# Optimization experiments

Hardware: AMD Instinct MI355X
Metric: run time of the kernel (lower is better)

The kernel has to match this reference:

```python
import jax, jax.numpy as jnp
import numpy as np

D_MODEL = 1024
HEADS = 16
D_K = D_MODEL // HEADS

def setup_inputs() -> dict:
    key = jax.random.key(0)
    ks = jax.random.split(key, 12)
    B, S = 4, 2048
    sc = 1.0 / np.sqrt(D_MODEL)
    inp = {
        'q': jax.random.normal(ks[0], (B, S, D_MODEL), jnp.float32),
        'k': jax.random.normal(ks[1], (B, S, D_MODEL), jnp.float32),
        'v': jax.random.normal(ks[2], (B, S, D_MODEL), jnp.float32),
        'mask': jnp.ones((B, S, S), jnp.int32),
        'Wq': jax.random.normal(ks[3], (D_MODEL, D_MODEL), jnp.float32) * sc,
        'bq': jnp.zeros((D_MODEL,), jnp.float32),
        'Wk': jax.random.normal(ks[4], (D_MODEL, D_MODEL), jnp.float32) * sc,
        'bk': jnp.zeros((D_MODEL,), jnp.float32),
        'Wv': jax.random.normal(ks[5], (D_MODEL, D_MODEL), jnp.float32) * sc,
        'bv': jnp.zeros((D_MODEL,), jnp.float32),
        'Wo': jax.random.normal(ks[6], (D_MODEL, D_MODEL), jnp.float32) * sc,
        'bo': jnp.zeros((D_MODEL,), jnp.float32),
    }
    return inp

def _proj_heads(x, W, b):
    # torch Linear: y = x @ W.T + b; then view(B,S,h,dk).transpose(1,2) -> [B,h,S,dk]
    B, S, _ = x.shape
    y = jnp.einsum('bsd,ed->bse', x, W) + b
    return y.reshape(B, S, HEADS, D_K).transpose(0, 2, 1, 3)

def reference(q, k, v, mask, Wq, bq, Wk, bk, Wv, bv, Wo, bo):
    B, S, _ = q.shape
    qh = _proj_heads(q, Wq, bq)  # [B,h,S,dk]
    kh = _proj_heads(k, Wk, bk)
    vh = _proj_heads(v, Wv, bv)
    scores = jnp.einsum('bhqd,bhkd->bhqk', qh, kh) / np.sqrt(D_K)
    scores = jnp.where(mask[:, None, :, :] == 0, jnp.float32(-1e9), scores)
    probs = jax.nn.softmax(scores, axis=-1)  # dropout = identity (eval mode)
    ctx = jnp.einsum('bhqk,bhkd->bhqd', probs, vh)
    concat = ctx.transpose(0, 2, 1, 3).reshape(B, S, D_MODEL)
    return jnp.einsum('bsd,ed->bse', concat, Wo) + bo
```

## Files before the change

kernel.cpp:

```cpp
#include <hip/hip_runtime.h>
#include <stdint.h>

#define DM 1024
#define SQL 2048
#define NB 4
#define NH 16
#define DK 64

typedef unsigned short u16;
typedef unsigned int u32;
typedef float f32x4 __attribute__((ext_vector_type(4)));
typedef short s16x8 __attribute__((ext_vector_type(8)));
typedef unsigned int u32x2 __attribute__((ext_vector_type(2)));

__device__ __forceinline__ u16 f2bf(float x) {
  union { float f; u32 u; } un; un.f = x;
  return (u16)((un.u + 0x8000u) >> 16);
}
__device__ __forceinline__ u32 pack_bf16(float a, float b) {
  union { float f; u32 u; } ua, ub; ua.f = a; ub.f = b;
  return ((ua.u + 0x8000u) >> 16) | ((ub.u + 0x8000u) & 0xFFFF0000u);
}

typedef __attribute__((address_space(3))) u32 lds_u32_t;
typedef __attribute__((address_space(1))) u32 g_u32_t;

__device__ __forceinline__ void async_cp16(void* lds, const void* g) {
  __builtin_amdgcn_global_load_lds((g_u32_t*)(unsigned long long)g,
                                   (lds_u32_t*)(unsigned long long)lds,
                                   16, 0, 0);
}

__device__ __forceinline__ void mfma16(f32x4& c, s16x8 a, s16x8 b) {
  c = __builtin_amdgcn_mfma_f32_16x16x32_bf16(a, b, c, 0, 0, 0);
}

__global__ void init_flag_k(int* flag) { if (threadIdx.x == 0) *flag = 1; }

__device__ __forceinline__ void store_bf4(u16* dst, float4 v) {
  u32 lo = pack_bf16(v.x, v.y);
  u32 hi = pack_bf16(v.z, v.w);
  ((u32*)dst)[0] = lo; ((u32*)dst)[1] = hi;
}

__global__ void __launch_bounds__(256) convert_scan_k(
    const float* __restrict__ q, const float* __restrict__ k, const float* __restrict__ v,
    const float* __restrict__ wq, const float* __restrict__ wk,
    const float* __restrict__ wv, const float* __restrict__ wo,
    const int* __restrict__ mask,
    u16* qb, u16* kb, u16* vb, u16* wqb, u16* wkb, u16* wvb, u16* wob, int* flag)
{
  const size_t i = (size_t)blockIdx.x * 256 + threadIdx.x;
  const size_t i4 = i * 4;
  store_bf4(qb + i4, *(const float4*)(q + i4));
  store_bf4(kb + i4, *(const float4*)(k + i4));
  store_bf4(vb + i4, *(const float4*)(v + i4));
  if (i4 < 1048576) {
    store_bf4(wqb + i4, *(const float4*)(wq + i4));
    store_bf4(wkb + i4, *(const float4*)(wk + i4));
    store_bf4(wvb + i4, *(const float4*)(wv + i4));
    store_bf4(wob + i4, *(const float4*)(wo + i4));
  }
  const size_t mi = i * 8;
  int4 m0 = *(const int4*)(mask + mi);
  int4 m1 = *(const int4*)(mask + mi + 4);
  bool z = (m0.x == 0) | (m0.y == 0) | (m0.z == 0) | (m0.w == 0) |
           (m1.x == 0) | (m1.y == 0) | (m1.z == 0) | (m1.w == 0);
  if (z) *flag = 0;
}

__device__ __forceinline__ void gemm_core(const u16* __restrict__ A, const u16* __restrict__ W,
                                          int m0, int n0, u16* sA, u16* sB, f32x4 (&acc)[4][4])
{
  const int tid = threadIdx.x;
  const int l = tid & 63, w = tid >> 6;
  const int g = l >> 4, ln = l & 15;
  const int wm = w & 1, wn = w >> 1;

  for (int kt = 0; kt < DM; kt += 64) {
#pragma unroll
    for (int i = 0; i < 4; ++i) {
      int s = w * 256 + i * 64 + l;
      int m = s >> 3;
      int kc = (s & 7) ^ (m & 7);
      async_cp16(sA + (size_t)(w * 256 + i * 64) * 8,
                 A + (size_t)(m0 + m) * DM + kt + kc * 8);
    }
#pragma unroll
    for (int i = 0; i < 4; ++i) {
      int s = w * 256 + i * 64 + l;
      int n = s >> 3;
      int kc = (s & 7) ^ (n & 7);
      async_cp16(sB + (size_t)(w * 256 + i * 64) * 8,
                 W + (size_t)(n0 + n) * DM + kt + kc * 8);
    }
    asm volatile("s_waitcnt vmcnt(0)" ::: "memory");
    __syncthreads();
#pragma unroll
    for (int ks = 0; ks < 2; ++ks) {
      s16x8 af[4], bfr[4];
#pragma unroll
      for (int mt = 0; mt < 4; ++mt) {
        int m = wm * 64 + mt * 16 + ln;
        int slot = m * 8 + ((ks * 4 + g) ^ (m & 7));
        af[mt] = *(const s16x8*)(sA + (size_t)slot * 8);
      }
#pragma unroll
      for (int nt = 0; nt < 4; ++nt) {
        int n = wn * 64 + nt * 16 + ln;
        int slot = n * 8 + ((ks * 4 + g) ^ (n & 7));
        bfr[nt] = *(const s16x8*)(sB + (size_t)slot * 8);
      }
#pragma unroll
      for (int mt = 0; mt < 4; ++mt)
#pragma unroll
        for (int nt = 0; nt < 4; ++nt)
          mfma16(acc[mt][nt], af[mt], bfr[nt]);
    }
    __syncthreads();
  }
}

__global__ void __launch_bounds__(256) gemm_qkv_k(
    const u16* __restrict__ qb, const u16* __restrict__ kb, const u16* __restrict__ vb,
    const u16* __restrict__ wqb, const u16* __restrict__ wkb, const u16* __restrict__ wvb,
    const float* __restrict__ bq, const float* __restrict__ bk, const float* __restrict__ bv,
    u16* Qh, u16* Kh, u16* Vt)
{
  __shared__ __align__(16) u16 sA[128 * 64];
  __shared__ __align__(16) u16 sB[128 * 64];
  const int z = blockIdx.z;
  const u16* A = (z == 0) ? qb : ((z == 1) ? kb : vb);
  const u16* W = (z == 0) ? wqb : ((z == 1) ? wkb : wvb);
  const float* bias = (z == 0) ? bq : ((z == 1) ? bk : bv);
  const int m0 = blockIdx.y * 128, n0 = blockIdx.x * 128;

  f32x4 zero4 = {0.f, 0.f, 0.f, 0.f};
  f32x4 acc[4][4];
#pragma unroll
  for (int mt = 0; mt < 4; ++mt)
#pragma unroll
    for (int nt = 0; nt < 4; ++nt) acc[mt][nt] = zero4;

  gemm_core(A, W, m0, n0, sA, sB, acc);

  const int tid = threadIdx.x;
  const int l = tid & 63, w = tid >> 6, g = l >> 4, ln = l & 15;
  const int wm = w & 1, wn = w >> 1;
  const float scale = (z == 0) ? (0.125f * 1.44269504089f) : 1.0f;
  u16* Crow = (z == 0) ? Qh : Kh;
#pragma unroll
  for (int nt = 0; nt < 4; ++nt) {
    int n = n0 + wn * 64 + nt * 16 + ln;
    float bn = bias[n];
#pragma unroll
    for (int mt = 0; mt < 4; ++mt) {
      int mb = m0 + wm * 64 + mt * 16 + g * 4;
      f32x4 vv = acc[mt][nt];
      if (z < 2) {
#pragma unroll
        for (int r = 0; r < 4; ++r)
          Crow[(size_t)(mb + r) * DM + n] = f2bf((vv[r] + bn) * scale);
      } else {
        int b = mb >> 11, s = mb & 2047;
        u32 lo = pack_bf16(vv[0] + bn, vv[1] + bn);
        u32 hi = pack_bf16(vv[2] + bn, vv[3] + bn);
        u32* dst = (u32*)(Vt + ((size_t)b << 21) + (size_t)n * SQL + s);
        dst[0] = lo; dst[1] = hi;
      }
    }
  }
}

__device__ __forceinline__ void p_transpose_frag(s16x8& out, u32 x0, u32 x1,
                                                 u32 y0, u32 y1,
                                                 int LA, int LB, bool ghi) {
  union { u32 wds[4]; s16x8 v; } pu;
#if __has_builtin(__builtin_amdgcn_permlane32_swap) && __has_builtin(__builtin_amdgcn_permlane16_swap)
  u32x2 r0 = __builtin_amdgcn_permlane32_swap(x0, y0, false, false);
  u32x2 s0 = __builtin_amdgcn_permlane16_swap(r0.x, r0.y, false, false);
  u32x2 r1 = __builtin_amdgcn_permlane32_swap(x1, y1, false, false);
  u32x2 s1 = __builtin_amdgcn_permlane16_swap(r1.x, r1.y, false, false);
  pu.wds[0] = s0.x; pu.wds[1] = s1.x; pu.wds[2] = s0.y; pu.wds[3] = s1.y;
#else
  u32 a0 = __shfl(x0, LA, 64), a1 = __shfl(x1, LA, 64);
  u32 b0 = __shfl(x0, LB, 64), b1 = __shfl(x1, LB, 64);
  u32 c0 = __shfl(y0, LA, 64), c1 = __shfl(y1, LA, 64);
  u32 d0 = __shfl(y0, LB, 64), d1 = __shfl(y1, LB, 64);
  pu.wds[0] = ghi ? c0 : a0;
  pu.wds[1] = ghi ? c1 : a1;
  pu.wds[2] = ghi ? d0 : b0;
  pu.wds[3] = ghi ? d1 : b1;
#endif
  out = pu.v;
}

__device__ __forceinline__ void attn_tile(
    const u16* Ks, const u16* Vs, int kv0,
    const s16x8 (&qf)[2][2], f32x4 (&ot)[4][2], f32x4 (&sums)[2],
    s16x8 ones, int allones, const int* __restrict__ mask,
    int b, int q0, int w, int g, int ln, int LA, int LB, bool ghi)
{
  f32x4 zero4 = {0.f, 0.f, 0.f, 0.f};
  __builtin_amdgcn_s_setprio(1);
#pragma unroll
  for (int kc = 0; kc < 2; ++kc) {
    f32x4 st[2][2];
#pragma unroll
    for (int t2 = 0; t2 < 2; ++t2)
#pragma unroll
      for (int u = 0; u < 2; ++u) st[t2][u] = zero4;
#pragma unroll
    for (int ks = 0; ks < 2; ++ks) {
#pragma unroll
      for (int t2 = 0; t2 < 2; ++t2) {
        int m = kc * 32 + t2 * 16 + ln;
        int slot = m * 8 + ((ks * 4 + g) ^ (m & 7));
        s16x8 kf = *(const s16x8*)(Ks + (size_t)slot * 8);
#pragma unroll
        for (int u = 0; u < 2; ++u) mfma16(st[t2][u], kf, qf[u][ks]);
      }
    }

    if (!allones) {
      const int* mb_ = mask + (size_t)b * SQL * SQL;
#pragma unroll
      for (int t2 = 0; t2 < 2; ++t2)
#pragma unroll
        for (int u = 0; u < 2; ++u)
#pragma unroll
          for (int r = 0; r < 4; ++r) {
            int kv = kv0 + kc * 32 + t2 * 16 + g * 4 + r;
            int qq = q0 + w * 32 + u * 16 + ln;
            if (mb_[(size_t)qq * SQL + kv] == 0) st[t2][u][r] = -30.f;
          }
    }

    s16x8 pf[2];
#pragma unroll
    for (int u = 0; u < 2; ++u) {
      u32 pkw[2][2];
#pragma unroll
      for (int t2 = 0; t2 < 2; ++t2) {
        float p0 = __builtin_amdgcn_exp2f(st[t2][u][0]);
        float p1 = __builtin_amdgcn_exp2f(st[t2][u][1]);
        float p2 = __builtin_amdgcn_exp2f(st[t2][u][2]);
        float p3 = __builtin_amdgcn_exp2f(st[t2][u][3]);
        pkw[t2][0] = pack_bf16(p0, p1);
        pkw[t2][1] = pack_bf16(p2, p3);
      }
      p_transpose_frag(pf[u], pkw[0][0], pkw[0][1], pkw[1][0], pkw[1][1], LA, LB, ghi);
      mfma16(sums[u], ones, pf[u]);
    }
#pragma unroll
    for (int mt = 0; mt < 4; ++mt) {
      int d = mt * 16 + ln;
      int slot = d * 8 + ((kc * 4 + g) ^ (d & 7));
      s16x8 vf = *(const s16x8*)(Vs + (size_t)slot * 8);
      mfma16(ot[mt][0], vf, pf[0]);
      mfma16(ot[mt][1], vf, pf[1]);
    }
  }
  __builtin_amdgcn_s_setprio(0);
}

__global__ void __launch_bounds__(256, 4) attn_k(
    const u16* __restrict__ Qh, const u16* __restrict__ Kh, const u16* __restrict__ Vt,
    const int* __restrict__ mask, const int* __restrict__ flag, u16* __restrict__ ctx)
{
  __shared__ __align__(16) u16 smem[17408];
  const int tid = threadIdx.x;
  const int l = tid & 63, w = tid >> 6, g = l >> 4, ln = l & 15;
  const int flat = blockIdx.x + 16 * (blockIdx.y + 16 * blockIdx.z);
  const int nid = (flat & 7) * 128 + (flat >> 3);
  const int q0 = (nid & 15) * 128;
  const int bh = nid >> 4;
  const int h = bh & 15, b = bh >> 4;
  const int allones = *flag;

  s16x8 qf[2][2];
#pragma unroll
  for (int u = 0; u < 2; ++u)
#pragma unroll
    for (int ks = 0; ks < 2; ++ks) {
      size_t row = (size_t)(b * SQL + q0 + w * 32 + u * 16 + ln);
      qf[u][ks] = *(const s16x8*)(Qh + row * DM + h * DK + ks * 32 + g * 8);
    }

  f32x4 zero4 = {0.f, 0.f, 0.f, 0.f};
  f32x4 ot[4][2];
#pragma unroll
  for (int mt = 0; mt < 4; ++mt)
#pragma unroll
    for (int u = 0; u < 2; ++u) ot[mt][u] = zero4;
  f32x4 sums[2];
  sums[0] = zero4; sums[1] = zero4;
  s16x8 ones;
#pragma unroll
  for (int i = 0; i < 8; ++i) ones[i] = (short)0x3F80;

  const int LA = (g & 1) * 32 + ln;
  const int LB = LA + 16;
  const bool ghi = (g >> 1) != 0;

  const int s0 = w * 128 + l, s1 = s0 + 64;
  const int m0r = s0 >> 3, m1r = s1 >> 3;
  const int c0 = ((s0 & 7) ^ (m0r & 7)) << 3;
  const int c1 = ((s1 & 7) ^ (m1r & 7)) << 3;
  const u16* gK0 = Kh + (size_t)(b * SQL + m0r) * DM + h * DK + c0;
  const u16* gK1 = Kh + (size_t)(b * SQL + m1r) * DM + h * DK + c1;
  const u16* gV0 = Vt + ((size_t)b << 21) + (size_t)(h * DK + m0r) * SQL + c0;
  const u16* gV1 = Vt + ((size_t)b << 21) + (size_t)(h * DK + m1r) * SQL + c1;
  u16* const dK = smem + (size_t)(w * 128) * 8;

#define STAGE_KV(BUFK, BUFV)                                           \
  do {                                                                 \
    async_cp16(dK + (BUFK), gK0);                                      \
    async_cp16(dK + (BUFK) + 512, gK1);                                \
    async_cp16(dK + (BUFV), gV0);                                      \
    async_cp16(dK + (BUFV) + 512, gV1);                                \
    gK0 += 64 * DM; gK1 += 64 * DM; gV0 += 64; gV1 += 64;              \
  } while (0)

  STAGE_KV(0, 4096);
  __syncthreads();

  for (int t = 0; t < 32; t += 2) {
    STAGE_KV(8192, 12288);
    attn_tile(smem, smem + 4096, t * 64, qf, ot, sums, ones, allones,
              mask, b, q0, w, g, ln, LA, LB, ghi);
    __syncthreads();
    if (t < 30) STAGE_KV(0, 4096);
    attn_tile(smem + 8192, smem + 12288, (t + 1) * 64, qf, ot, sums, ones,
              allones, mask, b, q0, w, g, ln, LA, LB, ghi);
    __syncthreads();
  }
#undef STAGE_KV

  float* red = (float*)smem;
#pragma unroll
  for (int u = 0; u < 2; ++u) {
    float inv = 1.0f / sums[u][0];
    int row = w * 32 + u * 16 + ln;
#pragma unroll
    for (int mt = 0; mt < 4; ++mt) {
      f32x4 vv = ot[mt][u] * inv;
      *(f32x4*)&red[(size_t)row * 68 + mt * 16 + g * 4] = vv;
    }
  }
  __syncthreads();
#pragma unroll
  for (int i = 0; i < 16; ++i) {
    int f2 = i * 256 + tid;
    int qq = f2 >> 5, dp = f2 & 31;
    float2 vv = *(const float2*)&red[(size_t)qq * 68 + dp * 2];
    u32 pkd = pack_bf16(vv.x, vv.y);
    *(u32*)(ctx + (size_t)(b * SQL + q0 + qq) * DM + h * DK + dp * 2) = pkd;
  }
}

__global__ void __launch_bounds__(256) gemm_out_k(
    const u16* __restrict__ ctx, const u16* __restrict__ wob,
    const float* __restrict__ bo, float* __restrict__ out)
{
  __shared__ __align__(16) u16 sA[128 * 64];
  __shared__ __align__(16) u16 sB[128 * 64];
  const int m0 = blockIdx.y * 128, n0 = blockIdx.x * 128;
  f32x4 zero4 = {0.f, 0.f, 0.f, 0.f};
  f32x4 acc[4][4];
#pragma unroll
  for (int mt = 0; mt < 4; ++mt)
#pragma unroll
    for (int nt = 0; nt < 4; ++nt) acc[mt][nt] = zero4;

  gemm_core(ctx, wob, m0, n0, sA, sB, acc);

  const int tid = threadIdx.x;
  const int l = tid & 63, w = tid >> 6, g = l >> 4, ln = l & 15;
  const int wm = w & 1, wn = w >> 1;
#pragma unroll
  for (int nt = 0; nt < 4; ++nt) {
    int n = n0 + wn * 64 + nt * 16 + ln;
    float bn = bo[n];
#pragma unroll
    for (int mt = 0; mt < 4; ++mt) {
      int mb = m0 + wm * 64 + mt * 16 + g * 4;
      f32x4 vv = acc[mt][nt];
#pragma unroll
      for (int r = 0; r < 4; ++r)
        out[(size_t)(mb + r) * DM + n] = vv[r] + bn;
    }
  }
}

extern "C" void kernel_launch(void* const* d_in, const int* in_sizes, int n_in,
                              void* d_out, int out_size, void* d_ws, size_t ws_size,
                              hipStream_t stream) {
  (void)in_sizes; (void)n_in; (void)out_size; (void)ws_size;
  const float* q  = (const float*)d_in[0];
  const float* k  = (const float*)d_in[1];
  const float* v  = (const float*)d_in[2];
  const int* mask = (const int*)d_in[3];
  const float* Wq = (const float*)d_in[4];
  const float* bq = (const float*)d_in[5];
  const float* Wk = (const float*)d_in[6];
  const float* bk = (const float*)d_in[7];
  const float* Wv = (const float*)d_in[8];
  const float* bv = (const float*)d_in[9];
  const float* Wo = (const float*)d_in[10];
  const float* bo = (const float*)d_in[11];
  float* out = (float*)d_out;
  char* ws = (char*)d_ws;

  u16* qb  = (u16*)(ws + 0);
  u16* kb  = (u16*)(ws + 16777216);
  u16* vb  = (u16*)(ws + 33554432);
  u16* Qh  = (u16*)(ws + 50331648);
  u16* Kh  = (u16*)(ws + 67108864);
  u16* Vt  = (u16*)(ws + 83886080);
  u16* ctx = (u16*)(ws + 100663296);
  u16* wqb = (u16*)(ws + 117440512);
  u16* wkb = (u16*)(ws + 119537664);
  u16* wvb = (u16*)(ws + 121634816);
  u16* wob = (u16*)(ws + 123731968);
  int* flag = (int*)(ws + 125829120);

  hipLaunchKernelGGL(init_flag_k, dim3(1), dim3(64), 0, stream, flag);
  hipLaunchKernelGGL(convert_scan_k, dim3(8192), dim3(256), 0, stream,
                     q, k, v, Wq, Wk, Wv, Wo, mask,
                     qb, kb, vb, wqb, wkb, wvb, wob, flag);
  hipLaunchKernelGGL(gemm_qkv_k, dim3(8, 64, 3), dim3(256), 0, stream,
                     qb, kb, vb, wqb, wkb, wvb, bq, bk, bv, Qh, Kh, Vt);
  hipLaunchKernelGGL(attn_k, dim3(16, 16, 4), dim3(256), 0, stream,
                     Qh, Kh, Vt, mask, flag, ctx);
  hipLaunchKernelGGL(gemm_out_k, dim3(8, 64), dim3(256), 0, stream,
                     ctx, wob, bo, out);
}
```

Baseline: 399.7 us.

## Use 256x256 double-buffered GEMM tiles with XCD-aware block mapping

Both projection GEMMs (QKV and output) move from 128x128 tiles with 256 threads to 256x256 tiles with 512 threads. Each warp now computes 128x64, and the LDS stage is double-buffered so the next K slice loads while the current one is multiplied. Block indices are remapped so neighbouring M tiles land on the same XCD, which is meant to improve L2 reuse of A rows and cut global traffic per FLOP. The cost is 128KB of LDS per block and larger accumulators (32 f32x4 per thread), which lowers occupancy and leaves fewer blocks (128 per z) to fill the CUs.

```diff
diff --git a/kernel.cpp b/kernel.cpp
--- a/kernel.cpp
+++ b/kernel.cpp
@@ -33,6 +33,13 @@
 
 __device__ __forceinline__ void mfma16(f32x4& c, s16x8 a, s16x8 b) {
   c = __builtin_amdgcn_mfma_f32_16x16x32_bf16(a, b, c, 0, 0, 0);
+}
+
+__device__ __forceinline__ void xcd_tile_map256(int j, int& m0, int& n0) {
+  const int xcd = j & 7;
+  const int idx = j >> 3;
+  m0 = (xcd * 4 + (idx >> 2)) * 256;
+  n0 = (idx & 3) * 256;
 }
 
 __global__ void init_flag_k(int* flag) { if (threadIdx.x == 0) *flag = 1; }
@@ -69,84 +76,107 @@
   if (z) *flag = 0;
 }
 
-__device__ __forceinline__ void gemm_core(const u16* __restrict__ A, const u16* __restrict__ W,
-                                          int m0, int n0, u16* sA, u16* sB, f32x4 (&acc)[4][4])
+__device__ __forceinline__ void gemm_stage256(const u16* __restrict__ A,
+                                              const u16* __restrict__ W,
+                                              int m0, int n0, int kt,
+                                              u16* sA, u16* sB, int tid, int w) {
+#pragma unroll
+  for (int i = 0; i < 4; ++i) {
+    int s = i * 512 + tid;
+    int m = s >> 3;
+    int kc = (s & 7) ^ (m & 7);
+    async_cp16(sA + (size_t)(i * 512 + w * 64) * 8,
+               A + (size_t)(m0 + m) * DM + kt + kc * 8);
+  }
+#pragma unroll
+  for (int i = 0; i < 4; ++i) {
+    int s = i * 512 + tid;
+    int n = s >> 3;
+    int kc = (s & 7) ^ (n & 7);
+    async_cp16(sB + (size_t)(i * 512 + w * 64) * 8,
+               W + (size_t)(n0 + n) * DM + kt + kc * 8);
+  }
+}
+
+__device__ __forceinline__ void gemm_compute256(const u16* sA, const u16* sB,
+                                                f32x4 (&acc)[8][4],
+                                                int wm, int wn, int g, int ln) {
+#pragma unroll
+  for (int ks = 0; ks < 2; ++ks) {
+    s16x8 af[8], bfr[4];
+#pragma unroll
+    for (int mt = 0; mt < 8; ++mt) {
+      int m = wm * 128 + mt * 16 + ln;
+      int slot = m * 8 + ((ks * 4 + g) ^ (m & 7));
+      af[mt] = *(const s16x8*)(sA + (size_t)slot * 8);
+    }
+#pragma unroll
+    for (int nt = 0; nt < 4; ++nt) {
+      int n = wn * 64 + nt * 16 + ln;
+      int slot = n * 8 + ((ks * 4 + g) ^ (n & 7));
+      bfr[nt] = *(const s16x8*)(sB + (size_t)slot * 8);
+    }
+#pragma unroll
+    for (int mt = 0; mt < 8; ++mt)
+#pragma unroll
+      for (int nt = 0; nt < 4; ++nt)
+        mfma16(acc[mt][nt], af[mt], bfr[nt]);
+  }
+}
+
+__device__ __forceinline__ void gemm_core256(const u16* __restrict__ A,
+                                             const u16* __restrict__ W,
+                                             int m0, int n0, u16* smem,
+                                             f32x4 (&acc)[8][4])
 {
   const int tid = threadIdx.x;
-  const int l = tid & 63, w = tid >> 6;
+  const int w = tid >> 6;
+  const int l = tid & 63;
   const int g = l >> 4, ln = l & 15;
-  const int wm = w & 1, wn = w >> 1;
-
-  for (int kt = 0; kt < DM; kt += 64) {
-#pragma unroll
-    for (int i = 0; i < 4; ++i) {
-      int s = w * 256 + i * 64 + l;
-      int m = s >> 3;
-      int kc = (s & 7) ^ (m & 7);
-      async_cp16(sA + (size_t)(w * 256 + i * 64) * 8,
-                 A + (size_t)(m0 + m) * DM + kt + kc * 8);
-    }
-#pragma unroll
-    for (int i = 0; i < 4; ++i) {
-      int s = w * 256 + i * 64 + l;
-      int n = s >> 3;
-      int kc = (s & 7) ^ (n & 7);
-      async_cp16(sB + (size_t)(w * 256 + i * 64) * 8,
-                 W + (size_t)(n0 + n) * DM + kt + kc * 8);
-    }
-    asm volatile("s_waitcnt vmcnt(0)" ::: "memory");
+  const int wm = w >> 2, wn = w & 3;
+  u16* sA0 = smem;
+  u16* sB0 = smem + 16384;
+  u16* sA1 = smem + 32768;
+  u16* sB1 = smem + 49152;
+
+  gemm_stage256(A, W, m0, n0, 0, sA0, sB0, tid, w);
+  __syncthreads();
+  for (int kt = 0; kt < DM; kt += 128) {
+    gemm_stage256(A, W, m0, n0, kt + 64, sA1, sB1, tid, w);
+    gemm_compute256(sA0, sB0, acc, wm, wn, g, ln);
     __syncthreads();
-#pragma unroll
-    for (int ks = 0; ks < 2; ++ks) {
-      s16x8 af[4], bfr[4];
-#pragma unroll
-      for (int mt = 0; mt < 4; ++mt) {
-        int m = wm * 64 + mt * 16 + ln;
-        int slot = m * 8 + ((ks * 4 + g) ^ (m & 7));
-        af[mt] = *(const s16x8*)(sA + (size_t)slot * 8);
-      }
-#pragma unroll
-      for (int nt = 0; nt < 4; ++nt) {
-        int n = wn * 64 + nt * 16 + ln;
-        int slot = n * 8 + ((ks * 4 + g) ^ (n & 7));
-        bfr[nt] = *(const s16x8*)(sB + (size_t)slot * 8);
-      }
-#pragma unroll
-      for (int mt = 0; mt < 4; ++mt)
-#pragma unroll
-        for (int nt = 0; nt < 4; ++nt)
-          mfma16(acc[mt][nt], af[mt], bfr[nt]);
-    }
+    if (kt + 128 < DM) gemm_stage256(A, W, m0, n0, kt + 128, sA0, sB0, tid, w);
+    gemm_compute256(sA1, sB1, acc, wm, wn, g, ln);
     __syncthreads();
   }
 }
 
-__global__ void __launch_bounds__(256) gemm_qkv_k(
+__global__ void __launch_bounds__(512, 2) gemm_qkv_k(
     const u16* __restrict__ qb, const u16* __restrict__ kb, const u16* __restrict__ vb,
     const u16* __restrict__ wqb, const u16* __restrict__ wkb, const u16* __restrict__ wvb,
     const float* __restrict__ bq, const float* __restrict__ bk, const float* __restrict__ bv,
     u16* Qh, u16* Kh, u16* Vt)
 {
-  __shared__ __align__(16) u16 sA[128 * 64];
-  __shared__ __align__(16) u16 sB[128 * 64];
+  __shared__ __align__(16) u16 smem[65536];
   const int z = blockIdx.z;
   const u16* A = (z == 0) ? qb : ((z == 1) ? kb : vb);
   const u16* W = (z == 0) ? wqb : ((z == 1) ? wkb : wvb);
   const float* bias = (z == 0) ? bq : ((z == 1) ? bk : bv);
-  const int m0 = blockIdx.y * 128, n0 = blockIdx.x * 128;
+  int m0, n0;
+  xcd_tile_map256(blockIdx.x + 4 * blockIdx.y, m0, n0);
 
   f32x4 zero4 = {0.f, 0.f, 0.f, 0.f};
-  f32x4 acc[4][4];
-#pragma unroll
-  for (int mt = 0; mt < 4; ++mt)
+  f32x4 acc[8][4];
+#pragma unroll
+  for (int mt = 0; mt < 8; ++mt)
 #pragma unroll
     for (int nt = 0; nt < 4; ++nt) acc[mt][nt] = zero4;
 
-  gemm_core(A, W, m0, n0, sA, sB, acc);
+  gemm_core256(A, W, m0, n0, smem, acc);
 
   const int tid = threadIdx.x;
   const int l = tid & 63, w = tid >> 6, g = l >> 4, ln = l & 15;
-  const int wm = w & 1, wn = w >> 1;
+  const int wm = w >> 2, wn = w & 3;
   const float scale = (z == 0) ? (0.125f * 1.44269504089f) : 1.0f;
   u16* Crow = (z == 0) ? Qh : Kh;
 #pragma unroll
@@ -154,8 +184,8 @@
     int n = n0 + wn * 64 + nt * 16 + ln;
     float bn = bias[n];
 #pragma unroll
-    for (int mt = 0; mt < 4; ++mt) {
-      int mb = m0 + wm * 64 + mt * 16 + g * 4;
+    for (int mt = 0; mt < 8; ++mt) {
+      int mb = m0 + wm * 128 + mt * 16 + g * 4;
       f32x4 vv = acc[mt][nt];
       if (z < 2) {
 #pragma unroll
@@ -359,32 +389,32 @@
   }
 }
 
-__global__ void __launch_bounds__(256) gemm_out_k(
+__global__ void __launch_bounds__(512, 2) gemm_out_k(
     const u16* __restrict__ ctx, const u16* __restrict__ wob,
     const float* __restrict__ bo, float* __restrict__ out)
 {
-  __shared__ __align__(16) u16 sA[128 * 64];
-  __shared__ __align__(16) u16 sB[128 * 64];
-  const int m0 = blockIdx.y * 128, n0 = blockIdx.x * 128;
+  __shared__ __align__(16) u16 smem[65536];
+  int m0, n0;
+  xcd_tile_map256(blockIdx.x + 4 * blockIdx.y, m0, n0);
   f32x4 zero4 = {0.f, 0.f, 0.f, 0.f};
-  f32x4 acc[4][4];
-#pragma unroll
-  for (int mt = 0; mt < 4; ++mt)
+  f32x4 acc[8][4];
+#pragma unroll
+  for (int mt = 0; mt < 8; ++mt)
 #pragma unroll
     for (int nt = 0; nt < 4; ++nt) acc[mt][nt] = zero4;
 
-  gemm_core(ctx, wob, m0, n0, sA, sB, acc);
+  gemm_core256(ctx, wob, m0, n0, smem, acc);
 
   const int tid = threadIdx.x;
   const int l = tid & 63, w = tid >> 6, g = l >> 4, ln = l & 15;
-  const int wm = w & 1, wn = w >> 1;
+  const int wm = w >> 2, wn = w & 3;
 #pragma unroll
   for (int nt = 0; nt < 4; ++nt) {
     int n = n0 + wn * 64 + nt * 16 + ln;
     float bn = bo[n];
 #pragma unroll
-    for (int mt = 0; mt < 4; ++mt) {
-      int mb = m0 + wm * 64 + mt * 16 + g * 4;
+    for (int mt = 0; mt < 8; ++mt) {
+      int mb = m0 + wm * 128 + mt * 16 + g * 4;
       f32x4 vv = acc[mt][nt];
 #pragma unroll
       for (int r = 0; r < 4; ++r)
@@ -429,10 +459,10 @@
   hipLaunchKernelGGL(convert_scan_k, dim3(8192), dim3(256), 0, stream,
                      q, k, v, Wq, Wk, Wv, Wo, mask,
                      qb, kb, vb, wqb, wkb, wvb, wob, flag);
-  hipLaunchKernelGGL(gemm_qkv_k, dim3(8, 64, 3), dim3(256), 0, stream,
+  hipLaunchKernelGGL(gemm_qkv_k, dim3(4, 32, 3), dim3(512), 0, stream,
                      qb, kb, vb, wqb, wkb, wvb, bq, bk, bv, Qh, Kh, Vt);
   hipLaunchKernelGGL(attn_k, dim3(16, 16, 4), dim3(256), 0, stream,
                      Qh, Kh, Vt, mask, flag, ctx);
-  hipLaunchKernelGGL(gemm_out_k, dim3(8, 64), dim3(256), 0, stream,
+  hipLaunchKernelGGL(gemm_out_k, dim3(4, 32), dim3(512), 0, stream,
                      ctx, wob, bo, out);
 }
```

Measured after the change: 443.0 us. 1.11x slower.
